# Kernel tuning notes

Hardware: AMD Instinct MI355X
Metric: run time of the kernel (lower is better)

The kernel has to match this reference:

```python
import jax, jax.numpy as jnp
import numpy as np

NEG_SLOPE = 0.2
EPS = 1e-6


def setup_inputs() -> dict:
    key = jax.random.key(0)
    k1, k2 = jax.random.split(key)
    B, C, N = 4, 64, 32768
    x = jax.random.normal(k1, (B, C, 3, N), dtype=jnp.float32)
    # VNLinear weight: nn.Linear(in, out, bias=False).weight -> [out, in]
    W = jax.random.normal(k2, (C, C), dtype=jnp.float32) * (1.0 / np.sqrt(C))
    return {"x": x, "W": W}


def reference(x, W):
    # VNLinear: kron(W, eye(3)) conv2d == per-3-vector channel mix
    # d[b,o,v,n] = sum_i W[o,i] * x[b,i,v,n]
    d = jnp.einsum('oi,bivn->bovn', W, x)
    dotprod = jnp.sum(x * d, axis=2, keepdims=True)      # [B,C,1,N]
    d_norm_sq = jnp.sum(d * d, axis=2, keepdims=True)    # [B,C,1,N]
    neg = x - (1.0 - NEG_SLOPE) * (dotprod / (d_norm_sq + EPS)) * d
    return jnp.where(dotprod >= 0, x, neg)
```

## Files before the change

### kernel.cpp

```cpp
#include <hip/hip_runtime.h>

#define NEG_SLOPE 0.2f
#define EPS 1e-6f


#define C_CH 64
#define V_DIM 3
#define N_FULL 32768
#define NT 64
#define THREADS 512

typedef __attribute__((ext_vector_type(8))) short bf16x8;
typedef __attribute__((ext_vector_type(4))) float f32x4;

__device__ __forceinline__ ushort f2bf(float f) {
    union { float f; unsigned u; } v; v.f = f;
    unsigned r = v.u + 0x7FFFu + ((v.u >> 16) & 1u);
    return (ushort)(r >> 16);
}
__device__ __forceinline__ float bf2f(ushort s) {
    union { unsigned u; float f; } v; v.u = ((unsigned)s) << 16; return v.f;
}
__device__ __forceinline__ unsigned pack_hl(float x) {
    union { float f; unsigned u; } a; a.f = x;
    unsigned t0 = a.u + 0x8000u;
    union { unsigned u; float f; } hb; hb.u = t0 & 0xffff0000u;
    union { float f; unsigned u; } rb; rb.f = x - hb.f;
    return __builtin_amdgcn_perm(t0, rb.u, 0x07060302u);
}
__device__ __forceinline__ float u2f(unsigned u) {
    union { unsigned u; float f; } v; v.u = u; return v.f;
}

__global__ void w_split_kernel(const float* __restrict__ W,
                               ushort* __restrict__ whi, ushort* __restrict__ wlo) {
    int i = blockIdx.x * 256 + threadIdx.x;
    if (i < C_CH * C_CH) {
        float w = W[i];
        ushort h = f2bf(w);
        whi[i] = h;
        wlo[i] = f2bf(w - bf2f(h));
    }
}

__device__ __forceinline__ int swz(int row) { return ((row >> 3) & 3) << 4; }

template<bool USE_WS>
__global__ __launch_bounds__(THREADS, 6)
void vn_mfma64(const float* __restrict__ x,
               const float* __restrict__ Wf,
               const ushort* __restrict__ whi, const ushort* __restrict__ wlo,
               float* __restrict__ out) {
    __shared__ unsigned xs[V_DIM * C_CH][NT];

    const int t    = threadIdx.x;
    const int tile = blockIdx.x;
    const int b    = tile >> 9;
    const int n0   = (tile & 511) << 6;

    const float* xb = x + (size_t)b * (C_CH * V_DIM * N_FULL) + n0;

    const int lane = t & 63;
    const int w    = t >> 6;
    const int wo   = w >> 2;
    const int wn   = w & 3;
    const int l4   = lane & 15;
    const int hi   = lane >> 4;

    bf16x8 Ah[2][2], Al[2][2];
    if (USE_WS) {
        #pragma unroll
        for (int m = 0; m < 2; ++m)
            #pragma unroll
            for (int kh = 0; kh < 2; ++kh) {
                size_t off = (size_t)(wo * 32 + m * 16 + l4) * C_CH + kh * 32 + hi * 8;
                Ah[m][kh] = *(const bf16x8*)(whi + off);
                Al[m][kh] = *(const bf16x8*)(wlo + off);
            }
    } else {
        #pragma unroll
        for (int m = 0; m < 2; ++m)
            #pragma unroll
            for (int kh = 0; kh < 2; ++kh) {
                const float* wp = Wf + (size_t)(wo * 32 + m * 16 + l4) * C_CH + kh * 32 + hi * 8;
                float4 wa = *(const float4*)wp;
                float4 wb = *(const float4*)(wp + 4);
                float wf[8] = {wa.x, wa.y, wa.z, wa.w, wb.x, wb.y, wb.z, wb.w};
                bf16x8 h, l;
                #pragma unroll
                for (int j = 0; j < 8; ++j) {
                    ushort hb = f2bf(wf[j]);
                    h[j] = (short)hb;
                    l[j] = (short)f2bf(wf[j] - bf2f(hb));
                }
                Ah[m][kh] = h; Al[m][kh] = l;
            }
    }

    #pragma unroll
    for (int it = 0; it < 6; ++it) {
        int idx = t + it * THREADS;
        int r   = idx >> 4;
        int c4  = (idx & 15) << 2;
        int i   = (r * 171) >> 9;
        int v   = r - 3 * i;
        int rowp = v * 64 + i;
        float4 vf4 = *(const float4*)(xb + (size_t)r * N_FULL + c4);
        float vf[4] = {vf4.x, vf4.y, vf4.z, vf4.w};
        unsigned p[4];
        #pragma unroll
        for (int q = 0; q < 4; ++q) p[q] = pack_hl(vf[q]);
        *(uint4*)&xs[rowp][c4 ^ swz(rowp)] = *(const uint4*)p;
    }
    __syncthreads();

    f32x4 acc[2][3];
    #pragma unroll
    for (int m = 0; m < 2; ++m)
        #pragma unroll
        for (int v = 0; v < 3; ++v)
            acc[m][v] = (f32x4){0.f, 0.f, 0.f, 0.f};

    const int acol = (wn * 16 + l4) ^ (hi << 4);
    #pragma unroll
    for (int v = 0; v < 3; ++v) {
        #pragma unroll
        for (int kh = 0; kh < 2; ++kh) {
            const int rowb = v * 64 + kh * 32 + hi * 8;
            unsigned p[8];
            #pragma unroll
            for (int j = 0; j < 8; ++j)
                p[j] = xs[rowb + j][acol];
            union { bf16x8 v8; unsigned d[4]; } BH, BL;
            #pragma unroll
            for (int q = 0; q < 4; ++q) {
                BH.d[q] = __builtin_amdgcn_perm(p[2 * q + 1], p[2 * q], 0x07060302u);
                BL.d[q] = __builtin_amdgcn_perm(p[2 * q + 1], p[2 * q], 0x05040100u);
            }
            #pragma unroll
            for (int m = 0; m < 2; ++m) {
                acc[m][v] = __builtin_amdgcn_mfma_f32_16x16x32_bf16(Ah[m][kh], BH.v8, acc[m][v], 0, 0, 0);
                acc[m][v] = __builtin_amdgcn_mfma_f32_16x16x32_bf16(Ah[m][kh], BL.v8, acc[m][v], 0, 0, 0);
                acc[m][v] = __builtin_amdgcn_mfma_f32_16x16x32_bf16(Al[m][kh], BH.v8, acc[m][v], 0, 0, 0);
            }
        }
    }

    const int n = wn * 16 + l4;
    float* ob = out + (size_t)b * (C_CH * V_DIM * N_FULL) + n0 + n;
    #pragma unroll
    for (int m = 0; m < 2; ++m) {
        #pragma unroll
        for (int r = 0; r < 4; ++r) {
            const int o = wo * 32 + m * 16 + hi * 4 + r;
            const int ecol = n ^ (((m * 2 + (hi >> 1)) & 3) << 4);
            float xv[3], dv[3];
            #pragma unroll
            for (int v = 0; v < 3; ++v) {
                unsigned p = xs[v * 64 + o][ecol];
                xv[v] = u2f(p & 0xffff0000u) + u2f(p << 16);
                dv[v] = acc[m][v][r];
            }
            float dot  = xv[0] * dv[0] + xv[1] * dv[1] + xv[2] * dv[2];
            float dnsq = dv[0] * dv[0] + dv[1] * dv[1] + dv[2] * dv[2];
            float f = (1.0f - NEG_SLOPE) * dot * __builtin_amdgcn_rcpf(dnsq + EPS);
            f = (dot >= 0.f) ? 0.f : f;
            float o0 = fmaf(-f, dv[0], xv[0]);
            float o1 = fmaf(-f, dv[1], xv[1]);
            float o2 = fmaf(-f, dv[2], xv[2]);
            float* op = ob + (size_t)o * (V_DIM * N_FULL);
            op[0 * N_FULL] = o0;
            op[1 * N_FULL] = o1;
            op[2 * N_FULL] = o2;
        }
    }
}

extern "C" void kernel_launch(void* const* d_in, const int* in_sizes, int n_in,
                              void* d_out, int out_size, void* d_ws, size_t ws_size,
                              hipStream_t stream) {
    const float* x = (const float*)d_in[0];
    const float* W = (const float*)d_in[1];
    float* out = (float*)d_out;

    const int B = 4;
    const int blocks = B * (N_FULL / NT);

    if (ws_size >= 2u * C_CH * C_CH * sizeof(ushort)) {
        ushort* whi = (ushort*)d_ws;
        ushort* wlo = whi + C_CH * C_CH;
        w_split_kernel<<<(C_CH * C_CH + 255) / 256, 256, 0, stream>>>(W, whi, wlo);
        vn_mfma64<true><<<blocks, THREADS, 0, stream>>>(x, W, whi, wlo, out);
    } else {
        vn_mfma64<false><<<blocks, THREADS, 0, stream>>>(x, W, nullptr, nullptr, out);
    }
}
```

Before: 43.60 us.

## Extract x in MFMA output layout via identity matmul, drop W split kernel

Removes the separate weight-splitting kernel launch and always converts W to hi/lo bf16 in-kernel. Issues all global x loads up front before the W conversion so the memory latency overlaps that setup work. Replaces the epilogue LDS reads of x with extra identity-matrix MFMAs that place x directly in the accumulator layout. This cuts LDS traffic and a launch, at the cost of extra MFMA work, more accumulator registers, and more live registers under the 6-waves-per-SIMD bound.

```diff
diff --git a/kernel.cpp b/kernel.cpp
--- a/kernel.cpp
+++ b/kernel.cpp
@@ -28,28 +28,12 @@
     union { float f; unsigned u; } rb; rb.f = x - hb.f;
     return __builtin_amdgcn_perm(t0, rb.u, 0x07060302u);
 }
-__device__ __forceinline__ float u2f(unsigned u) {
-    union { unsigned u; float f; } v; v.u = u; return v.f;
-}
-
-__global__ void w_split_kernel(const float* __restrict__ W,
-                               ushort* __restrict__ whi, ushort* __restrict__ wlo) {
-    int i = blockIdx.x * 256 + threadIdx.x;
-    if (i < C_CH * C_CH) {
-        float w = W[i];
-        ushort h = f2bf(w);
-        whi[i] = h;
-        wlo[i] = f2bf(w - bf2f(h));
-    }
-}
 
 __device__ __forceinline__ int swz(int row) { return ((row >> 3) & 3) << 4; }
 
-template<bool USE_WS>
 __global__ __launch_bounds__(THREADS, 6)
 void vn_mfma64(const float* __restrict__ x,
                const float* __restrict__ Wf,
-               const ushort* __restrict__ whi, const ushort* __restrict__ wlo,
                float* __restrict__ out) {
     __shared__ unsigned xs[V_DIM * C_CH][NT];
 
@@ -67,34 +51,44 @@
     const int l4   = lane & 15;
     const int hi   = lane >> 4;
 
+    float4 xr[6];
+    #pragma unroll
+    for (int it = 0; it < 6; ++it) {
+        int idx = t + it * THREADS;
+        int r   = idx >> 4;
+        int c4  = (idx & 15) << 2;
+        xr[it] = *(const float4*)(xb + (size_t)r * N_FULL + c4);
+    }
+
     bf16x8 Ah[2][2], Al[2][2];
-    if (USE_WS) {
+    #pragma unroll
+    for (int m = 0; m < 2; ++m)
         #pragma unroll
-        for (int m = 0; m < 2; ++m)
+        for (int kh = 0; kh < 2; ++kh) {
+            const float* wp = Wf + (size_t)(wo * 32 + m * 16 + l4) * C_CH + kh * 32 + hi * 8;
+            float4 wa = *(const float4*)wp;
+            float4 wb = *(const float4*)(wp + 4);
+            float wf[8] = {wa.x, wa.y, wa.z, wa.w, wb.x, wb.y, wb.z, wb.w};
+            bf16x8 h, l;
             #pragma unroll
-            for (int kh = 0; kh < 2; ++kh) {
-                size_t off = (size_t)(wo * 32 + m * 16 + l4) * C_CH + kh * 32 + hi * 8;
-                Ah[m][kh] = *(const bf16x8*)(whi + off);
-                Al[m][kh] = *(const bf16x8*)(wlo + off);
+            for (int j = 0; j < 8; ++j) {
+                ushort hb = f2bf(wf[j]);
+                h[j] = (short)hb;
+                l[j] = (short)f2bf(wf[j] - bf2f(hb));
             }
-    } else {
+            Ah[m][kh] = h; Al[m][kh] = l;
+        }
+
+    bf16x8 Aid0, Aid1;
+    {
+        const int j1 = l4 & 7;
+        const bool h0 = (hi == (l4 >> 3));
+        const bool h1 = (hi == 2 + (l4 >> 3));
         #pragma unroll
-        for (int m = 0; m < 2; ++m)
-            #pragma unroll
-            for (int kh = 0; kh < 2; ++kh) {
-                const float* wp = Wf + (size_t)(wo * 32 + m * 16 + l4) * C_CH + kh * 32 + hi * 8;
-                float4 wa = *(const float4*)wp;
-                float4 wb = *(const float4*)(wp + 4);
-                float wf[8] = {wa.x, wa.y, wa.z, wa.w, wb.x, wb.y, wb.z, wb.w};
-                bf16x8 h, l;
-                #pragma unroll
-                for (int j = 0; j < 8; ++j) {
-                    ushort hb = f2bf(wf[j]);
-                    h[j] = (short)hb;
-                    l[j] = (short)f2bf(wf[j] - bf2f(hb));
-                }
-                Ah[m][kh] = h; Al[m][kh] = l;
-            }
+        for (int j = 0; j < 8; ++j) {
+            Aid0[j] = (short)((h0 && j == j1) ? 0x3F80 : 0);
+            Aid1[j] = (short)((h1 && j == j1) ? 0x3F80 : 0);
+        }
     }
 
     #pragma unroll
@@ -105,8 +99,7 @@
         int i   = (r * 171) >> 9;
         int v   = r - 3 * i;
         int rowp = v * 64 + i;
-        float4 vf4 = *(const float4*)(xb + (size_t)r * N_FULL + c4);
-        float vf[4] = {vf4.x, vf4.y, vf4.z, vf4.w};
+        float vf[4] = {xr[it].x, xr[it].y, xr[it].z, xr[it].w};
         unsigned p[4];
         #pragma unroll
         for (int q = 0; q < 4; ++q) p[q] = pack_hl(vf[q]);
@@ -114,12 +107,14 @@
     }
     __syncthreads();
 
-    f32x4 acc[2][3];
+    f32x4 acc[2][3], accx[2][3];
     #pragma unroll
     for (int m = 0; m < 2; ++m)
         #pragma unroll
-        for (int v = 0; v < 3; ++v)
-            acc[m][v] = (f32x4){0.f, 0.f, 0.f, 0.f};
+        for (int v = 0; v < 3; ++v) {
+            acc[m][v]  = (f32x4){0.f, 0.f, 0.f, 0.f};
+            accx[m][v] = (f32x4){0.f, 0.f, 0.f, 0.f};
+        }
 
     const int acol = (wn * 16 + l4) ^ (hi << 4);
     #pragma unroll
@@ -143,6 +138,12 @@
                 acc[m][v] = __builtin_amdgcn_mfma_f32_16x16x32_bf16(Ah[m][kh], BL.v8, acc[m][v], 0, 0, 0);
                 acc[m][v] = __builtin_amdgcn_mfma_f32_16x16x32_bf16(Al[m][kh], BH.v8, acc[m][v], 0, 0, 0);
             }
+            if (kh == wo) {
+                accx[0][v] = __builtin_amdgcn_mfma_f32_16x16x32_bf16(Aid0, BH.v8, accx[0][v], 0, 0, 0);
+                accx[0][v] = __builtin_amdgcn_mfma_f32_16x16x32_bf16(Aid0, BL.v8, accx[0][v], 0, 0, 0);
+                accx[1][v] = __builtin_amdgcn_mfma_f32_16x16x32_bf16(Aid1, BH.v8, accx[1][v], 0, 0, 0);
+                accx[1][v] = __builtin_amdgcn_mfma_f32_16x16x32_bf16(Aid1, BL.v8, accx[1][v], 0, 0, 0);
+            }
         }
     }
 
@@ -153,12 +154,10 @@
         #pragma unroll
         for (int r = 0; r < 4; ++r) {
             const int o = wo * 32 + m * 16 + hi * 4 + r;
-            const int ecol = n ^ (((m * 2 + (hi >> 1)) & 3) << 4);
             float xv[3], dv[3];
             #pragma unroll
             for (int v = 0; v < 3; ++v) {
-                unsigned p = xs[v * 64 + o][ecol];
-                xv[v] = u2f(p & 0xffff0000u) + u2f(p << 16);
+                xv[v] = accx[m][v][r];
                 dv[v] = acc[m][v][r];
             }
             float dot  = xv[0] * dv[0] + xv[1] * dv[1] + xv[2] * dv[2];
@@ -185,13 +184,5 @@
 
     const int B = 4;
     const int blocks = B * (N_FULL / NT);
-
-    if (ws_size >= 2u * C_CH * C_CH * sizeof(ushort)) {
-        ushort* whi = (ushort*)d_ws;
-        ushort* wlo = whi + C_CH * C_CH;
-        w_split_kernel<<<(C_CH * C_CH + 255) / 256, 256, 0, stream>>>(W, whi, wlo);
-        vn_mfma64<true><<<blocks, THREADS, 0, stream>>>(x, W, whi, wlo, out);
-    } else {
-        vn_mfma64<false><<<blocks, THREADS, 0, stream>>>(x, W, nullptr, nullptr, out);
-    }
+    vn_mfma64<<<blocks, THREADS, 0, stream>>>(x, W, out);
 }
```

Result: slower. 68.58 us (+57.3%).

## Load x tile directly into LDS via global_load_lds and split hi/lo at read

Applied to the files above, without the earlier changes.

Replaces the register-staged global load, which packed each float into a hi/lo bf16 pair before writing to shared memory, with direct global-to-LDS DMA loads of raw fp32 into a natural row layout with an XOR chunk swizzle. The hi/lo bf16 split is now computed when the MFMA B operands are read from LDS. The x loads are also issued before the weight fragments are loaded, so the two overlap. This removes VGPR staging and conversion work from the load phase, in exchange for extra ALU work in the MFMA loop and a different LDS bank-access pattern.

```diff
diff --git a/kernel.cpp b/kernel.cpp
--- a/kernel.cpp
+++ b/kernel.cpp
@@ -21,12 +21,8 @@
 __device__ __forceinline__ float bf2f(ushort s) {
     union { unsigned u; float f; } v; v.u = ((unsigned)s) << 16; return v.f;
 }
-__device__ __forceinline__ unsigned pack_hl(float x) {
-    union { float f; unsigned u; } a; a.f = x;
-    unsigned t0 = a.u + 0x8000u;
-    union { unsigned u; float f; } hb; hb.u = t0 & 0xffff0000u;
-    union { float f; unsigned u; } rb; rb.f = x - hb.f;
-    return __builtin_amdgcn_perm(t0, rb.u, 0x07060302u);
+__device__ __forceinline__ unsigned f2u(float f) {
+    union { float f; unsigned u; } v; v.f = f; return v.u;
 }
 __device__ __forceinline__ float u2f(unsigned u) {
     union { unsigned u; float f; } v; v.u = u; return v.f;
@@ -43,15 +39,13 @@
     }
 }
 
-__device__ __forceinline__ int swz(int row) { return ((row >> 3) & 3) << 4; }
-
 template<bool USE_WS>
 __global__ __launch_bounds__(THREADS, 6)
-void vn_mfma64(const float* __restrict__ x,
-               const float* __restrict__ Wf,
-               const ushort* __restrict__ whi, const ushort* __restrict__ wlo,
-               float* __restrict__ out) {
-    __shared__ unsigned xs[V_DIM * C_CH][NT];
+void vn_dma64(const float* __restrict__ x,
+              const float* __restrict__ Wf,
+              const ushort* __restrict__ whi, const ushort* __restrict__ wlo,
+              float* __restrict__ out) {
+    __shared__ float xs[V_DIM * C_CH][NT];
 
     const int t    = threadIdx.x;
     const int tile = blockIdx.x;
@@ -66,6 +60,18 @@
     const int wn   = w & 3;
     const int l4   = lane & 15;
     const int hi   = lane >> 4;
+
+    #pragma unroll
+    for (int it = 0; it < 6; ++it) {
+        int r = 4 * (w * 6 + it) + (lane >> 4);
+        int i = (r * 171) >> 9;
+        int chunk = (lane & 15) ^ (((i >> 3) & 3) << 2);
+        const float* g = xb + (size_t)r * N_FULL + (chunk << 2);
+        void* l = (char*)(&xs[0][0]) + (size_t)(w * 6 + it) * 1024 + (size_t)lane * 16;
+        __builtin_amdgcn_global_load_lds(
+            (const __attribute__((address_space(1))) unsigned*)g,
+            (__attribute__((address_space(3))) unsigned*)l, 16, 0, 0);
+    }
 
     bf16x8 Ah[2][2], Al[2][2];
     if (USE_WS) {
@@ -97,21 +103,6 @@
             }
     }
 
-    #pragma unroll
-    for (int it = 0; it < 6; ++it) {
-        int idx = t + it * THREADS;
-        int r   = idx >> 4;
-        int c4  = (idx & 15) << 2;
-        int i   = (r * 171) >> 9;
-        int v   = r - 3 * i;
-        int rowp = v * 64 + i;
-        float4 vf4 = *(const float4*)(xb + (size_t)r * N_FULL + c4);
-        float vf[4] = {vf4.x, vf4.y, vf4.z, vf4.w};
-        unsigned p[4];
-        #pragma unroll
-        for (int q = 0; q < 4; ++q) p[q] = pack_hl(vf[q]);
-        *(uint4*)&xs[rowp][c4 ^ swz(rowp)] = *(const uint4*)p;
-    }
     __syncthreads();
 
     f32x4 acc[2][3];
@@ -126,16 +117,20 @@
     for (int v = 0; v < 3; ++v) {
         #pragma unroll
         for (int kh = 0; kh < 2; ++kh) {
-            const int rowb = v * 64 + kh * 32 + hi * 8;
-            unsigned p[8];
+            const int ib = kh * 32 + hi * 8;
+            float f[8];
             #pragma unroll
             for (int j = 0; j < 8; ++j)
-                p[j] = xs[rowb + j][acol];
+                f[j] = xs[3 * (ib + j) + v][acol];
             union { bf16x8 v8; unsigned d[4]; } BH, BL;
+            unsigned rl[8];
+            #pragma unroll
+            for (int j = 0; j < 8; ++j)
+                rl[j] = f2u(f[j] - u2f(f2u(f[j]) & 0xffff0000u));
             #pragma unroll
             for (int q = 0; q < 4; ++q) {
-                BH.d[q] = __builtin_amdgcn_perm(p[2 * q + 1], p[2 * q], 0x07060302u);
-                BL.d[q] = __builtin_amdgcn_perm(p[2 * q + 1], p[2 * q], 0x05040100u);
+                BH.d[q] = __builtin_amdgcn_perm(f2u(f[2 * q + 1]), f2u(f[2 * q]), 0x07060302u);
+                BL.d[q] = __builtin_amdgcn_perm(rl[2 * q + 1], rl[2 * q], 0x07060302u);
             }
             #pragma unroll
             for (int m = 0; m < 2; ++m) {
@@ -151,15 +146,14 @@
     #pragma unroll
     for (int m = 0; m < 2; ++m) {
         #pragma unroll
-        for (int r = 0; r < 4; ++r) {
-            const int o = wo * 32 + m * 16 + hi * 4 + r;
+        for (int rr = 0; rr < 4; ++rr) {
+            const int o = wo * 32 + m * 16 + hi * 4 + rr;
             const int ecol = n ^ (((m * 2 + (hi >> 1)) & 3) << 4);
             float xv[3], dv[3];
             #pragma unroll
             for (int v = 0; v < 3; ++v) {
-                unsigned p = xs[v * 64 + o][ecol];
-                xv[v] = u2f(p & 0xffff0000u) + u2f(p << 16);
-                dv[v] = acc[m][v][r];
+                xv[v] = xs[3 * o + v][ecol];
+                dv[v] = acc[m][v][rr];
             }
             float dot  = xv[0] * dv[0] + xv[1] * dv[1] + xv[2] * dv[2];
             float dnsq = dv[0] * dv[0] + dv[1] * dv[1] + dv[2] * dv[2];
@@ -190,8 +184,8 @@
         ushort* whi = (ushort*)d_ws;
         ushort* wlo = whi + C_CH * C_CH;
         w_split_kernel<<<(C_CH * C_CH + 255) / 256, 256, 0, stream>>>(W, whi, wlo);
-        vn_mfma64<true><<<blocks, THREADS, 0, stream>>>(x, W, whi, wlo, out);
+        vn_dma64<true><<<blocks, THREADS, 0, stream>>>(x, W, whi, wlo, out);
     } else {
-        vn_mfma64<false><<<blocks, THREADS, 0, stream>>>(x, W, nullptr, nullptr, out);
+        vn_dma64<false><<<blocks, THREADS, 0, stream>>>(x, W, nullptr, nullptr, out);
     }
 }
```

Result: slower. 46.32 us (+6.2%).
